# Kernel optimization log

Hardware: AMD Instinct MI355X
Metric: run time of the kernel (lower is better)

## Reference

```python
import jax, jax.numpy as jnp
import numpy as np

B, T, D, H = 4, 4096, 1280, 5120  # batch, tokens (64x64 SAM grid), embedding_dim, mlp_dim


def setup_inputs() -> dict:
    key = jax.random.key(0)
    k = jax.random.split(key, 5)
    # int8 quantized activations and weights (symmetric, per-tensor)
    x = jax.random.randint(k[0], (B, T, D), -128, 128, dtype=jnp.int8)
    w1 = jax.random.randint(k[1], (H, D), -128, 128, dtype=jnp.int8)  # lin1.weight [out,in]
    b1 = jax.random.normal(k[2], (H,), jnp.float32) * 0.02            # fp32 bias
    w2 = jax.random.randint(k[3], (D, H), -128, 128, dtype=jnp.int8)  # lin2.weight [out,in]
    b2 = jax.random.normal(k[4], (D,), jnp.float32) * 0.02
    a1 = jnp.float32(0.05 * 0.01)   # input_scale * w1_scale (dequant alpha of lin1)
    s_req = jnp.float32(0.08)       # lin2_input_scale (requant scale after GELU)
    a2 = jnp.float32(0.08 * 0.01)   # lin2_input_scale * w2_scale (dequant alpha of lin2)
    return dict(x=x, w1=w1, b1=b1, w2=w2, b2=b2, a1=a1, s_req=s_req, a2=a2)


def reference(x, w1, b1, w2, b2, a1, s_req, a2):
    acc1 = jnp.einsum('btd,hd->bth', x.astype(jnp.int32), w1.astype(jnp.int32))
    h = acc1.astype(jnp.float32) * a1 + b1              # [B,T,H] fp32
    # exact (erf) GELU, then requantize to int8 for lin2's input
    g = jax.nn.gelu(h, approximate=False)
    q = jnp.clip(jnp.round(g / s_req), -128, 127).astype(jnp.int8)
    acc2 = jnp.einsum('bth,dh->btd', q.astype(jnp.int32), w2.astype(jnp.int32))
    return acc2.astype(jnp.float32) * a2 + b2           # [B,T,D] fp32
```

## Files before the change

kernel.cpp:

```cpp
#include <hip/hip_runtime.h>
#include <stdint.h>
#include <math.h>

typedef __attribute__((ext_vector_type(4))) int i32x4;
typedef __attribute__((ext_vector_type(16))) int i32x16;
typedef __attribute__((ext_vector_type(4))) float f32x4;

constexpr int D_DIM = 1280;
constexpr int H_DIM = 5120;

__device__ __forceinline__ void gload_lds16(const void* g, void* l) {
  __builtin_amdgcn_global_load_lds(
      (const __attribute__((address_space(1))) void*)g,
      (__attribute__((address_space(3))) void*)l,
      16, 0, 0);
}

__device__ __forceinline__ float gelu_fast(float h) {
  const float x = h * 0.70710678118f;
  const float ax = fabsf(x);
  const float t = __frcp_rn(__builtin_fmaf(0.3275911f, ax, 1.0f));
  float p = __builtin_fmaf(1.061405429f, t, -1.453152027f);
  p = __builtin_fmaf(p, t, 1.421413741f);
  p = __builtin_fmaf(p, t, -0.284496736f);
  p = __builtin_fmaf(p, t, 0.254829592f);
  p *= t;
  const float e = __expf(-x * x);
  const float erf_ax = __builtin_fmaf(-p, e, 1.0f);
  const float erf_x = copysignf(erf_ax, x);
  return 0.5f * h * (1.0f + erf_x);
}

__global__ void __launch_bounds__(256) k_packw(const int* __restrict__ s1,
                                               const int* __restrict__ s2,
                                               int8_t* __restrict__ out,
                                               long wn) {
  long i = ((long)blockIdx.x * 256 + threadIdx.x) * 16;
  const int* p = (i < wn) ? (s1 + i) : (s2 + (i - wn));
  i32x4 a = *(const i32x4*)(p);
  i32x4 b = *(const i32x4*)(p + 4);
  i32x4 c = *(const i32x4*)(p + 8);
  i32x4 d = *(const i32x4*)(p + 12);
  i32x4 r;
  r.x = (a.x & 255) | ((a.y & 255) << 8) | ((a.z & 255) << 16) | (a.w << 24);
  r.y = (b.x & 255) | ((b.y & 255) << 8) | ((b.z & 255) << 16) | (b.w << 24);
  r.z = (c.x & 255) | ((c.y & 255) << 8) | ((c.z & 255) << 16) | (c.w << 24);
  r.w = (d.x & 255) | ((d.y & 255) << 8) | ((d.z & 255) << 16) | (d.w << 24);
  *(i32x4*)(out + i) = r;
}

__global__ void __launch_bounds__(256) k_pack(const int* __restrict__ in,
                                              int8_t* __restrict__ out,
                                              long n) {
  long i = ((long)blockIdx.x * 256 + threadIdx.x) * 16;
  if (i >= n) return;
  const int* p = in + i;
  i32x4 a = *(const i32x4*)(p);
  i32x4 b = *(const i32x4*)(p + 4);
  i32x4 c = *(const i32x4*)(p + 8);
  i32x4 d = *(const i32x4*)(p + 12);
  i32x4 r;
  r.x = (a.x & 255) | ((a.y & 255) << 8) | ((a.z & 255) << 16) | (a.w << 24);
  r.y = (b.x & 255) | ((b.y & 255) << 8) | ((b.z & 255) << 16) | (b.w << 24);
  r.z = (c.x & 255) | ((c.y & 255) << 8) | ((c.z & 255) << 16) | (c.w << 24);
  r.w = (d.x & 255) | ((d.y & 255) << 8) | ((d.z & 255) << 16) | (d.w << 24);
  *(i32x4*)(out + i) = r;
}

template <int KDIM, int NDIM, bool GELU>
__global__ void __launch_bounds__(256, 2)
k_gemm(const int8_t* __restrict__ A, const int8_t* __restrict__ B,
       const float* __restrict__ bias, const float* __restrict__ ps1,
       const float* __restrict__ ps2, void* __restrict__ Cout, int Mtiles) {
  constexpr int BM = 128, BN = 128, BKB = 128;
  constexpr int NT = KDIM / BKB;
  constexpr int BNC = NDIM / BN;
  constexpr int G = BNC * 4;

  __shared__ __align__(16) int8_t smem[4 * 16384];

  const int nwg = Mtiles * BNC;
  int bm, bn;
  {
    const int bid = blockIdx.x;
    const int q = nwg >> 3, r = nwg & 7, x = bid & 7, l = bid >> 3;
    const int swz = (x < r ? x * (q + 1) : r * (q + 1) + (x - r) * q) + l;
    if ((Mtiles & 3) == 0) {
      const int g = swz / G, rr = swz % G;
      bn = rr >> 2;
      bm = g * 4 + (rr & 3);
    } else {
      bn = swz % BNC;
      bm = swz / BNC;
    }
  }

  const int tid = threadIdx.x;
  const int lane = tid & 63, wid = tid >> 6;
  const int wr = wid >> 1, wc = wid & 1;

  const int srow = tid >> 3;
  const int soff = (((tid & 7) ^ (srow & 7)) << 4);
  const int8_t* Ath = A + (size_t)(bm * BM + srow) * KDIM + soff;
  const int8_t* Bth = B + (size_t)(bn * BN + srow) * KDIM + soff;
  const int dT = tid * 16;

  auto STAGE = [&](int boff, const int8_t* ga, const int8_t* gb) {
#pragma unroll
    for (int p = 0; p < 4; ++p)
      gload_lds16(ga + (size_t)(p * 32) * KDIM, smem + boff + dT + p * 4096);
#pragma unroll
    for (int p = 0; p < 4; ++p)
      gload_lds16(gb + (size_t)(p * 32) * KDIM,
                  smem + 32768 + boff + dT + p * 4096);
  };

  const int r32 = lane & 31, hi5 = lane >> 5;
  const int fsw = (lane & 7) << 4;
  const int kq = hi5 << 4;
  const int8_t* aP[4];
  const int8_t* bP[4];
#pragma unroll
  for (int ks = 0; ks < 4; ++ks) {
    const int koff = (ks * 32 + kq) ^ fsw;
    aP[ks] = smem + (wr * 64 + r32) * BKB + koff;
    bP[ks] = smem + 32768 + (wc * 64 + r32) * BKB + koff;
  }

  i32x16 acc[2][2] = {};

  auto COMPUTE = [&](int boff) {
#pragma unroll
    for (int ks = 0; ks < 4; ++ks) {
      i32x4 a0 = *(const i32x4*)(aP[ks] + boff);
      i32x4 a1 = *(const i32x4*)(aP[ks] + boff + 4096);
      i32x4 b0 = *(const i32x4*)(bP[ks] + boff);
      i32x4 b1 = *(const i32x4*)(bP[ks] + boff + 4096);
      if constexpr (GELU) {
        acc[0][0] = __builtin_amdgcn_mfma_i32_32x32x32_i8(b0, a0, acc[0][0], 0, 0, 0);
        acc[0][1] = __builtin_amdgcn_mfma_i32_32x32x32_i8(b0, a1, acc[0][1], 0, 0, 0);
        acc[1][0] = __builtin_amdgcn_mfma_i32_32x32x32_i8(b1, a0, acc[1][0], 0, 0, 0);
        acc[1][1] = __builtin_amdgcn_mfma_i32_32x32x32_i8(b1, a1, acc[1][1], 0, 0, 0);
      } else {
        acc[0][0] = __builtin_amdgcn_mfma_i32_32x32x32_i8(a0, b0, acc[0][0], 0, 0, 0);
        acc[0][1] = __builtin_amdgcn_mfma_i32_32x32x32_i8(a0, b1, acc[0][1], 0, 0, 0);
        acc[1][0] = __builtin_amdgcn_mfma_i32_32x32x32_i8(a1, b0, acc[1][0], 0, 0, 0);
        acc[1][1] = __builtin_amdgcn_mfma_i32_32x32x32_i8(a1, b1, acc[1][1], 0, 0, 0);
      }
    }
  };

  STAGE(0, Ath, Bth);
  __syncthreads();
  const int8_t* gA = Ath + BKB;
  const int8_t* gB = Bth + BKB;
#pragma unroll 1
  for (int t = 0; t < NT; t += 2) {
    STAGE(16384, gA, gB);
    COMPUTE(0);
    __syncthreads();
    if (t + 2 < NT) STAGE(0, gA + BKB, gB + BKB);
    COMPUTE(16384);
    __syncthreads();
    gA += 2 * BKB;
    gB += 2 * BKB;
  }

  if constexpr (GELU) {
    const float s1 = *ps1;
    const float rs = 1.0f / (*ps2);
    int8_t* Q = (int8_t*)Cout;
    int8_t* lb = smem;
#pragma unroll
    for (int n = 0; n < 2; ++n) {
#pragma unroll
      for (int q = 0; q < 4; ++q) {
        const int hl = wc * 64 + n * 32 + q * 8 + hi5 * 4;
        const f32x4 bv = *(const f32x4*)(bias + bn * BN + hl);
#pragma unroll
        for (int m = 0; m < 2; ++m) {
          uint32_t pk = 0;
#pragma unroll
          for (int rr = 0; rr < 4; ++rr) {
            const float h = __builtin_fmaf((float)acc[n][m][q * 4 + rr], s1, bv[rr]);
            float qf = rintf(gelu_fast(h) * rs);
            qf = fminf(127.0f, fmaxf(-128.0f, qf));
            pk |= ((uint32_t)((int)qf & 255)) << (rr * 8);
          }
          const int row = wr * 64 + m * 32 + r32;
          const int ad = row * 128 + ((((hl >> 4) ^ (row & 7)) << 4)) + (hl & 12);
          *(uint32_t*)(lb + ad) = pk;
        }
      }
    }
    __syncthreads();
#pragma unroll
    for (int it = 0; it < 4; ++it) {
      const int row = wid * 32 + it * 8 + (lane >> 3);
      const int sl = lane & 7;
      i32x4 v = *(const i32x4*)(lb + row * 128 + ((sl ^ (row & 7)) << 4));
      *(i32x4*)(Q + (size_t)(bm * BM + row) * NDIM + bn * BN + sl * 16) = v;
    }
  } else {
    const float s1 = *ps1;
    float* O = (float*)Cout;
    const int colb = bn * BN + wc * 64 + r32;
#pragma unroll
    for (int n = 0; n < 2; ++n) {
      const int col = colb + n * 32;
      const float bv = bias[col];
#pragma unroll
      for (int m = 0; m < 2; ++m) {
        const int rowb = bm * BM + wr * 64 + m * 32 + hi5 * 4;
#pragma unroll
        for (int q = 0; q < 4; ++q)
#pragma unroll
          for (int rr = 0; rr < 4; ++rr) {
            const int row = rowb + q * 8 + rr;
            O[(size_t)row * NDIM + col] =
                __builtin_fmaf((float)acc[m][n][q * 4 + rr], s1, bv);
          }
      }
    }
  }
}

extern "C" void kernel_launch(void* const* d_in, const int* in_sizes, int n_in,
                              void* d_out, int out_size, void* d_ws, size_t ws_size,
                              hipStream_t stream) {
  (void)in_sizes; (void)n_in; (void)out_size;
  const int*   x32  = (const int*)d_in[0];
  const int*   w132 = (const int*)d_in[1];
  const float* b1   = (const float*)d_in[2];
  const int*   w232 = (const int*)d_in[3];
  const float* b2   = (const float*)d_in[4];
  const float* a1   = (const float*)d_in[5];
  const float* sreq = (const float*)d_in[6];
  const float* a2   = (const float*)d_in[7];
  float* out = (float*)d_out;

  const int M = 4 * 4096;
  const size_t WN = (size_t)H_DIM * D_DIM;
  constexpr int BM = 128, BN = 128;

  int8_t* w1p  = (int8_t*)d_ws;
  int8_t* w2p  = w1p + WN;
  int8_t* base = w2p + WN;

  size_t avail = ws_size > 2 * WN ? ws_size - 2 * WN : 0;
  size_t rows = avail / (size_t)(D_DIM + H_DIM);
  int Mc = (int)((rows / BM) * BM);
  if (Mc > M) Mc = M;
  if (Mc < BM) Mc = BM;

  k_packw<<<(int)(2 * WN / 4096), 256, 0, stream>>>(w132, w232, w1p, (long)WN);

  for (int m0 = 0; m0 < M; m0 += Mc) {
    const int mc = (M - m0 < Mc) ? (M - m0) : Mc;
    int8_t* xp = base;
    int8_t* q  = base + (size_t)Mc * D_DIM;
    const size_t nx = (size_t)mc * D_DIM;
    const int mt = mc / BM;
    k_pack<<<(int)(nx / 4096), 256, 0, stream>>>(x32 + (size_t)m0 * D_DIM, xp, (long)nx);
    k_gemm<D_DIM, H_DIM, true><<<mt * (H_DIM / BN), 256, 0, stream>>>(
        xp, w1p, b1, a1, sreq, q, mt);
    k_gemm<H_DIM, D_DIM, false><<<mt * (D_DIM / BN), 256, 0, stream>>>(
        q, w2p, b2, a2, nullptr, out + (size_t)m0 * D_DIM, mt);
  }
}
```

Before: 314.9 us.

## Switch both int8 GEMMs to 256x256 tiles with 512-thread workgroups

Replaces the 128x128, 256-thread GEMM with a 256x256 tile kernel using 8 waves, each computing a 128x64 sub-tile (4x2 MFMA 32x32x32 blocks). Each LDS fragment load now feeds more MFMAs and global traffic per output is halved. It also adds s_setprio around the MFMA bursts and changes the tile ordering for the two GEMMs. For lin1 the operands are swapped so weights supply the row dimension. In exchange it uses 128 KB of LDS, more accumulator registers and fewer workgroups, which limits occupancy and wave-level parallelism.

```diff
diff --git a/kernel.cpp b/kernel.cpp
--- a/kernel.cpp
+++ b/kernel.cpp
@@ -67,103 +67,92 @@
   *(i32x4*)(out + i) = r;
 }
 
-template <int KDIM, int NDIM, bool GELU>
-__global__ void __launch_bounds__(256, 2)
-k_gemm(const int8_t* __restrict__ A, const int8_t* __restrict__ B,
-       const float* __restrict__ bias, const float* __restrict__ ps1,
-       const float* __restrict__ ps2, void* __restrict__ Cout, int Mtiles) {
-  constexpr int BM = 128, BN = 128, BKB = 128;
+template <int KDIM, int ODIM, bool GELU, bool CFAST>
+__global__ void __launch_bounds__(512, 2)
+k_gemm256(const int8_t* __restrict__ P, const int8_t* __restrict__ S,
+          const float* __restrict__ bias, const float* __restrict__ ps1,
+          const float* __restrict__ ps2, void* __restrict__ Cout,
+          int rtiles, int ctiles) {
+  constexpr int BKB = 128;
   constexpr int NT = KDIM / BKB;
-  constexpr int BNC = NDIM / BN;
-  constexpr int G = BNC * 4;
-
-  __shared__ __align__(16) int8_t smem[4 * 16384];
-
-  const int nwg = Mtiles * BNC;
-  int bm, bn;
+  __shared__ __align__(16) int8_t smem[131072];
+
+  const int nwg = rtiles * ctiles;
+  int rt, ct;
   {
     const int bid = blockIdx.x;
     const int q = nwg >> 3, r = nwg & 7, x = bid & 7, l = bid >> 3;
     const int swz = (x < r ? x * (q + 1) : r * (q + 1) + (x - r) * q) + l;
-    if ((Mtiles & 3) == 0) {
-      const int g = swz / G, rr = swz % G;
-      bn = rr >> 2;
-      bm = g * 4 + (rr & 3);
-    } else {
-      bn = swz % BNC;
-      bm = swz / BNC;
-    }
+    if (CFAST) { rt = swz / ctiles; ct = swz % ctiles; }
+    else       { ct = swz / rtiles; rt = swz % rtiles; }
   }
 
   const int tid = threadIdx.x;
   const int lane = tid & 63, wid = tid >> 6;
-  const int wr = wid >> 1, wc = wid & 1;
+  const int wr = wid >> 2, wc = wid & 3;
+  const int r32 = lane & 31, hi5 = lane >> 5;
 
   const int srow = tid >> 3;
-  const int soff = (((tid & 7) ^ (srow & 7)) << 4);
-  const int8_t* Ath = A + (size_t)(bm * BM + srow) * KDIM + soff;
-  const int8_t* Bth = B + (size_t)(bn * BN + srow) * KDIM + soff;
+  const int soff = ((tid & 7) ^ (srow & 7)) << 4;
+  const int8_t* Pth = P + (size_t)(rt * 256 + srow) * KDIM + soff;
+  const int8_t* Sth = S + (size_t)(ct * 256 + srow) * KDIM + soff;
   const int dT = tid * 16;
 
-  auto STAGE = [&](int boff, const int8_t* ga, const int8_t* gb) {
+  auto STAGE = [&](int buf, int t) {
+    const int8_t* gp = Pth + t * BKB;
+    const int8_t* gs = Sth + t * BKB;
 #pragma unroll
     for (int p = 0; p < 4; ++p)
-      gload_lds16(ga + (size_t)(p * 32) * KDIM, smem + boff + dT + p * 4096);
+      gload_lds16(gp + (size_t)(p * 64) * KDIM, smem + buf * 32768 + dT + p * 8192);
 #pragma unroll
     for (int p = 0; p < 4; ++p)
-      gload_lds16(gb + (size_t)(p * 32) * KDIM,
-                  smem + 32768 + boff + dT + p * 4096);
+      gload_lds16(gs + (size_t)(p * 64) * KDIM,
+                  smem + 65536 + buf * 32768 + dT + p * 8192);
   };
 
-  const int r32 = lane & 31, hi5 = lane >> 5;
-  const int fsw = (lane & 7) << 4;
+  const int fsw = (r32 & 7) << 4;
   const int kq = hi5 << 4;
-  const int8_t* aP[4];
-  const int8_t* bP[4];
-#pragma unroll
-  for (int ks = 0; ks < 4; ++ks) {
-    const int koff = (ks * 32 + kq) ^ fsw;
-    aP[ks] = smem + (wr * 64 + r32) * BKB + koff;
-    bP[ks] = smem + 32768 + (wc * 64 + r32) * BKB + koff;
-  }
-
-  i32x16 acc[2][2] = {};
-
-  auto COMPUTE = [&](int boff) {
+  int koff[4];
+#pragma unroll
+  for (int ks = 0; ks < 4; ++ks) koff[ks] = (ks * 32 + kq) ^ fsw;
+  const int prow = (wr * 128 + r32) * BKB;
+  const int srw  = (wc * 64 + r32) * BKB;
+
+  i32x16 acc[4][2] = {};
+
+  auto COMPUTE = [&](int buf) {
+    const int8_t* Pb = smem + buf * 32768;
+    const int8_t* Sb = smem + 65536 + buf * 32768;
 #pragma unroll
     for (int ks = 0; ks < 4; ++ks) {
-      i32x4 a0 = *(const i32x4*)(aP[ks] + boff);
-      i32x4 a1 = *(const i32x4*)(aP[ks] + boff + 4096);
-      i32x4 b0 = *(const i32x4*)(bP[ks] + boff);
-      i32x4 b1 = *(const i32x4*)(bP[ks] + boff + 4096);
-      if constexpr (GELU) {
-        acc[0][0] = __builtin_amdgcn_mfma_i32_32x32x32_i8(b0, a0, acc[0][0], 0, 0, 0);
-        acc[0][1] = __builtin_amdgcn_mfma_i32_32x32x32_i8(b0, a1, acc[0][1], 0, 0, 0);
-        acc[1][0] = __builtin_amdgcn_mfma_i32_32x32x32_i8(b1, a0, acc[1][0], 0, 0, 0);
-        acc[1][1] = __builtin_amdgcn_mfma_i32_32x32x32_i8(b1, a1, acc[1][1], 0, 0, 0);
-      } else {
-        acc[0][0] = __builtin_amdgcn_mfma_i32_32x32x32_i8(a0, b0, acc[0][0], 0, 0, 0);
-        acc[0][1] = __builtin_amdgcn_mfma_i32_32x32x32_i8(a0, b1, acc[0][1], 0, 0, 0);
-        acc[1][0] = __builtin_amdgcn_mfma_i32_32x32x32_i8(a1, b0, acc[1][0], 0, 0, 0);
-        acc[1][1] = __builtin_amdgcn_mfma_i32_32x32x32_i8(a1, b1, acc[1][1], 0, 0, 0);
-      }
+      i32x4 pf[4], sf[2];
+#pragma unroll
+      for (int i = 0; i < 4; ++i)
+        pf[i] = *(const i32x4*)(Pb + prow + i * 4096 + koff[ks]);
+#pragma unroll
+      for (int j = 0; j < 2; ++j)
+        sf[j] = *(const i32x4*)(Sb + srw + j * 4096 + koff[ks]);
+      __builtin_amdgcn_s_setprio(1);
+#pragma unroll
+      for (int i = 0; i < 4; ++i)
+#pragma unroll
+        for (int j = 0; j < 2; ++j)
+          acc[i][j] =
+              __builtin_amdgcn_mfma_i32_32x32x32_i8(pf[i], sf[j], acc[i][j], 0, 0, 0);
+      __builtin_amdgcn_s_setprio(0);
     }
   };
 
-  STAGE(0, Ath, Bth);
+  STAGE(0, 0);
   __syncthreads();
-  const int8_t* gA = Ath + BKB;
-  const int8_t* gB = Bth + BKB;
 #pragma unroll 1
   for (int t = 0; t < NT; t += 2) {
-    STAGE(16384, gA, gB);
+    STAGE(1, t + 1);
     COMPUTE(0);
     __syncthreads();
-    if (t + 2 < NT) STAGE(0, gA + BKB, gB + BKB);
-    COMPUTE(16384);
+    if (t + 2 < NT) STAGE(0, t + 2);
+    COMPUTE(1);
     __syncthreads();
-    gA += 2 * BKB;
-    gB += 2 * BKB;
   }
 
   if constexpr (GELU) {
@@ -172,53 +161,51 @@
     int8_t* Q = (int8_t*)Cout;
     int8_t* lb = smem;
 #pragma unroll
-    for (int n = 0; n < 2; ++n) {
+    for (int i = 0; i < 4; ++i) {
 #pragma unroll
       for (int q = 0; q < 4; ++q) {
-        const int hl = wc * 64 + n * 32 + q * 8 + hi5 * 4;
-        const f32x4 bv = *(const f32x4*)(bias + bn * BN + hl);
-#pragma unroll
-        for (int m = 0; m < 2; ++m) {
+        const int hl = wr * 128 + i * 32 + q * 8 + hi5 * 4;
+        const f32x4 bv = *(const f32x4*)(bias + rt * 256 + hl);
+#pragma unroll
+        for (int j = 0; j < 2; ++j) {
+          const int tok = wc * 64 + j * 32 + r32;
           uint32_t pk = 0;
 #pragma unroll
           for (int rr = 0; rr < 4; ++rr) {
-            const float h = __builtin_fmaf((float)acc[n][m][q * 4 + rr], s1, bv[rr]);
+            const float h = __builtin_fmaf((float)acc[i][j][q * 4 + rr], s1, bv[rr]);
             float qf = rintf(gelu_fast(h) * rs);
             qf = fminf(127.0f, fmaxf(-128.0f, qf));
             pk |= ((uint32_t)((int)qf & 255)) << (rr * 8);
           }
-          const int row = wr * 64 + m * 32 + r32;
-          const int ad = row * 128 + ((((hl >> 4) ^ (row & 7)) << 4)) + (hl & 12);
+          const int ad = tok * 256 + ((((hl >> 4) ^ (tok & 7)) << 4)) + (hl & 12);
           *(uint32_t*)(lb + ad) = pk;
         }
       }
     }
     __syncthreads();
 #pragma unroll
-    for (int it = 0; it < 4; ++it) {
-      const int row = wid * 32 + it * 8 + (lane >> 3);
-      const int sl = lane & 7;
-      i32x4 v = *(const i32x4*)(lb + row * 128 + ((sl ^ (row & 7)) << 4));
-      *(i32x4*)(Q + (size_t)(bm * BM + row) * NDIM + bn * BN + sl * 16) = v;
+    for (int it = 0; it < 8; ++it) {
+      const int row = (tid >> 4) + it * 32;
+      const int sl = tid & 15;
+      i32x4 v = *(const i32x4*)(lb + row * 256 + ((sl ^ (row & 7)) << 4));
+      *(i32x4*)(Q + (size_t)(ct * 256 + row) * ODIM + rt * 256 + sl * 16) = v;
     }
   } else {
     const float s1 = *ps1;
     float* O = (float*)Cout;
-    const int colb = bn * BN + wc * 64 + r32;
-#pragma unroll
-    for (int n = 0; n < 2; ++n) {
-      const int col = colb + n * 32;
-      const float bv = bias[col];
-#pragma unroll
-      for (int m = 0; m < 2; ++m) {
-        const int rowb = bm * BM + wr * 64 + m * 32 + hi5 * 4;
+#pragma unroll
+    for (int i = 0; i < 4; ++i) {
+#pragma unroll
+      for (int j = 0; j < 2; ++j) {
+        const int col = ct * 256 + wc * 64 + j * 32 + r32;
+        const float bv = bias[col];
 #pragma unroll
         for (int q = 0; q < 4; ++q)
 #pragma unroll
           for (int rr = 0; rr < 4; ++rr) {
-            const int row = rowb + q * 8 + rr;
-            O[(size_t)row * NDIM + col] =
-                __builtin_fmaf((float)acc[m][n][q * 4 + rr], s1, bv);
+            const int row = rt * 256 + wr * 128 + i * 32 + q * 8 + hi5 * 4 + rr;
+            O[(size_t)row * ODIM + col] =
+                __builtin_fmaf((float)acc[i][j][q * 4 + rr], s1, bv);
           }
       }
     }
@@ -241,7 +228,7 @@
 
   const int M = 4 * 4096;
   const size_t WN = (size_t)H_DIM * D_DIM;
-  constexpr int BM = 128, BN = 128;
+  constexpr int BT = 256;
 
   int8_t* w1p  = (int8_t*)d_ws;
   int8_t* w2p  = w1p + WN;
@@ -249,9 +236,9 @@
 
   size_t avail = ws_size > 2 * WN ? ws_size - 2 * WN : 0;
   size_t rows = avail / (size_t)(D_DIM + H_DIM);
-  int Mc = (int)((rows / BM) * BM);
+  int Mc = (int)((rows / BT) * BT);
   if (Mc > M) Mc = M;
-  if (Mc < BM) Mc = BM;
+  if (Mc < BT) Mc = BT;
 
   k_packw<<<(int)(2 * WN / 4096), 256, 0, stream>>>(w132, w232, w1p, (long)WN);
 
@@ -260,11 +247,11 @@
     int8_t* xp = base;
     int8_t* q  = base + (size_t)Mc * D_DIM;
     const size_t nx = (size_t)mc * D_DIM;
-    const int mt = mc / BM;
+    const int mt = mc / BT;
     k_pack<<<(int)(nx / 4096), 256, 0, stream>>>(x32 + (size_t)m0 * D_DIM, xp, (long)nx);
-    k_gemm<D_DIM, H_DIM, true><<<mt * (H_DIM / BN), 256, 0, stream>>>(
-        xp, w1p, b1, a1, sreq, q, mt);
-    k_gemm<H_DIM, D_DIM, false><<<mt * (D_DIM / BN), 256, 0, stream>>>(
-        q, w2p, b2, a2, nullptr, out + (size_t)m0 * D_DIM, mt);
-  }
-}
+    k_gemm256<D_DIM, H_DIM, true, true><<<20 * mt, 512, 0, stream>>>(
+        w1p, xp, b1, a1, sreq, q, 20, mt);
+    k_gemm256<H_DIM, D_DIM, false, false><<<mt * 5, 512, 0, stream>>>(
+        q, w2p, b2, a2, a2, out + (size_t)m0 * D_DIM, mt, 5);
+  }
+}
```

Result: slower. 365.0 us (+15.9%).
